# Kernel tuning notes

Hardware: AMD Instinct MI355X
Metric: run time of the kernel (lower is better)

Reference implementation:

```python
import jax, jax.numpy as jnp
import numpy as np

B, C, L = 4, 64, 4096
RED = 4          # reduction -> q/k channels = C // RED = 16
N_HASHES = 4
HASH_BUCKETS = min(L // 4, 32)  # = 32, matches torch code
EPS = 1e-5


def _conv1x1(x, W, b):
    # x: [B, Cin, L], W: [Cout, Cin], b: [Cout]
    return jnp.einsum('bcl,oc->bol', x, W) + b[None, :, None]


def setup_inputs() -> dict:
    key = jax.random.key(0)
    ks = jax.random.split(key, 12)
    Cq = C // RED
    x = jax.random.normal(ks[0], (B, C, L), dtype=jnp.float32)
    hash_idx = jax.random.randint(ks[1], (B, N_HASHES, L), 0, HASH_BUCKETS, dtype=jnp.int32)
    sC = 1.0 / np.sqrt(C)
    Wq = jax.random.normal(ks[2], (Cq, C), dtype=jnp.float32) * sC
    bq = jax.random.normal(ks[3], (Cq,), dtype=jnp.float32) * 0.01
    Wk = jax.random.normal(ks[4], (Cq, C), dtype=jnp.float32) * sC
    bk = jax.random.normal(ks[5], (Cq,), dtype=jnp.float32) * 0.01
    Wv = jax.random.normal(ks[6], (C, C), dtype=jnp.float32) * sC
    bv = jax.random.normal(ks[7], (C,), dtype=jnp.float32) * 0.01
    Wo = jax.random.normal(ks[8], (C, C), dtype=jnp.float32) * sC
    bo = jax.random.normal(ks[9], (C,), dtype=jnp.float32) * 0.01
    gamma = jax.random.normal(ks[10], (1,), dtype=jnp.float32)  # nonzero so attn path matters
    bn_w = jnp.ones((C,), dtype=jnp.float32)
    bn_b = jnp.zeros((C,), dtype=jnp.float32)
    return dict(x=x, hash_idx=hash_idx, Wq=Wq, bq=bq, Wk=Wk, bk=bk,
                Wv=Wv, bv=bv, Wo=Wo, bo=bo, gamma=gamma, bn_w=bn_w, bn_b=bn_b)


def reference(x, hash_idx, Wq, bq, Wk, bk, Wv, bv, Wo, bo, gamma, bn_w, bn_b):
    # 1x1 conv projections
    q = _conv1x1(x, Wq, bq)   # [B, C/RED, L]
    k = _conv1x1(x, Wk, bk)   # [B, C/RED, L]
    v = _conv1x1(x, Wv, bv)   # [B, C, L]

    qT = q.transpose(0, 2, 1)  # [B, L, Cq]
    kT = k.transpose(0, 2, 1)
    vT = v.transpose(0, 2, 1)  # [B, L, C]

    # raw scores are hash-independent; only the bucket mask changes per hash
    scores = jnp.einsum('bic,bjc->bij', qT, kT)  # [B, L, L], no sqrt(d) scaling (matches torch)

    n_hashes = hash_idx.shape[1]
    acc = jnp.zeros_like(vT)
    for h in range(n_hashes):  # small fixed loop
        idx = hash_idx[:, h, :]                       # [B, L]
        mask = idx[:, :, None] == idx[:, None, :]     # same-bucket mask [B, L, L]
        s = jnp.where(mask, scores, -1e9)
        attn = jax.nn.softmax(s, axis=-1)             # within-bucket softmax (diag always valid)
        acc = acc + jnp.einsum('bij,bjc->bic', attn, vT)
    attn_out = (acc / n_hashes).transpose(0, 2, 1)    # [B, C, L], averaged over hashes

    out = _conv1x1(attn_out, Wo, bo)
    out = gamma * out + x                             # residual with learned scalar

    # BatchNorm1d, training mode: biased batch stats over (B, L) per channel
    mean = out.mean(axis=(0, 2), keepdims=True)
    var = out.var(axis=(0, 2), keepdims=True)
    out = (out - mean) * jax.lax.rsqrt(var + EPS)
    out = out * bn_w[None, :, None] + bn_b[None, :, None]
    return out
```

## Files before the change

kernel.cpp:

```cpp
#include <hip/hip_runtime.h>
#include <math.h>

#define Bn 4
#define Cn 64
#define Ln 4096
#define CQ 16
#define NH 4
#define NB 32
#define EPSV 1e-5f

#define MAXS 384
#define CH2 64
#define KSTR 20
#define VSTR 64

#define QSZ   (Bn*Ln*CQ)
#define VSZ   (Bn*Ln*Cn)
#define ACCSZ (Bn*Ln*Cn)
#define NBH   (Bn*NH)

#define OFF_K   QSZ
#define OFF_V   (2*QSZ)
#define OFF_ACC (2*QSZ + VSZ)

#define LOG2E 1.44269504088896f

__global__ __launch_bounds__(256) void proj_kernel(
        const float* __restrict__ x,
        const float* __restrict__ Wq, const float* __restrict__ bq,
        const float* __restrict__ Wk, const float* __restrict__ bk,
        const float* __restrict__ Wv, const float* __restrict__ bv,
        float* __restrict__ q, float* __restrict__ k, float* __restrict__ v) {
    __shared__ float sWt[Cn*32];
    __shared__ float sb[32];
    int tid = threadIdx.x;
    int third = blockIdx.x % 3;
    int pg    = blockIdx.x / 3;
    int rbase = third * 32;
    for (int idx = tid; idx < Cn*32; idx += 256) {
        int rr = idx & 31, c = idx >> 5;
        int r = rbase + rr;
        float w;
        if (r < 16)      w = Wq[r*Cn + c];
        else if (r < 32) w = Wk[(r-16)*Cn + c];
        else             w = Wv[(r-32)*Cn + c];
        sWt[c*32 + rr] = w;
    }
    if (tid < 32) {
        int r = rbase + tid;
        sb[tid] = (r < 16) ? bq[r] : (r < 32 ? bk[r-16] : bv[r-32]);
    }
    __syncthreads();
    int p = tid & 63, og = tid >> 6;
    int gp = pg * 64 + p;
    int b = gp >> 12, l = gp & (Ln - 1);
    const float* xp = &x[b*Cn*Ln + l];
    int rr0 = og * 8;
    float val[8];
    #pragma unroll
    for (int i = 0; i < 8; i++) val[i] = sb[rr0 + i];
    #pragma unroll
    for (int c0 = 0; c0 < Cn; c0 += 8) {
        float xv[8];
        #pragma unroll
        for (int i = 0; i < 8; i++) xv[i] = xp[(c0 + i)*Ln];
        #pragma unroll
        for (int i = 0; i < 8; i++) {
            const float* wrow = &sWt[(c0 + i)*32 + rr0];
            #pragma unroll
            for (int j = 0; j < 8; j++) val[j] = fmaf(wrow[j], xv[i], val[j]);
        }
    }
    int f = third*8 + og*2;
    float4 t0 = make_float4(val[0], val[1], val[2], val[3]);
    float4 t1 = make_float4(val[4], val[5], val[6], val[7]);
    float4* q4 = (float4*)&q[gp*CQ];
    float4* k4 = (float4*)&k[gp*CQ];
    float4* v4 = (float4*)&v[gp*Cn];
    if (f < 4)      { q4[f]   = t0; q4[f+1] = t1; }
    else if (f < 8) { k4[f-4] = t0; k4[f-3] = t1; }
    else            { v4[f-8] = t0; v4[f-7] = t1; }
}

template<int NS, int MODE>
__device__ __forceinline__ void attn_pass(
        int qbase, int S, int b, int h, int tid, int rem,
        const int* list, float* ks, float* vs,
        const float* __restrict__ q, const float* __restrict__ k,
        const float* __restrict__ v, float* __restrict__ acc) {
    int qd = tid >> 2, c4 = tid & 3;
    float4 qr[NS][4];
    float4 o[NS][4];
    float lsum[NS];
    int qi[NS], iqr[NS];
    #pragma unroll
    for (int s = 0; s < NS; s++) {
        qi[s] = qbase + 64*s + qd;
        iqr[s] = 0;
        lsum[s] = 0.f;
        #pragma unroll
        for (int i = 0; i < 4; i++) o[s][i] = make_float4(0.f,0.f,0.f,0.f);
        if (qi[s] < S) {
            iqr[s] = list[qi[s]];
            const float4* qp = (const float4*)&q[(b*Ln + iqr[s])*CQ];
            #pragma unroll
            for (int i = 0; i < 4; i++) {
                float4 t = qp[i];
                t.x*=LOG2E; t.y*=LOG2E; t.z*=LOG2E; t.w*=LOG2E;
                qr[s][i] = t;
            }
        } else {
            #pragma unroll
            for (int i = 0; i < 4; i++) qr[s][i] = make_float4(0.f,0.f,0.f,0.f);
        }
    }
    for (int cc = 0; cc < S; cc += CH2) {
        int nk = min(CH2, S - cc);
        __syncthreads();
        {
            int jj = tid >> 2, cf = tid & 3;
            if (jj < nk) {
                const float4* kp = (const float4*)&k[(b*Ln + list[cc+jj])*CQ];
                *(float4*)&ks[jj*KSTR + cf*4] = kp[cf];
            }
        }
        #pragma unroll
        for (int uu = 0; uu < 4; uu++) {
            int idx = uu*256 + tid;
            int jj = idx >> 4, cf = idx & 15;
            if (jj < nk) {
                const float4* vp = (const float4*)&v[(b*Ln + list[cc+jj])*Cn];
                *(float4*)&vs[jj*VSTR + cf*4] = vp[cf];
            }
        }
        __syncthreads();
        if (rem > 0) {
            for (int j = 0; j < nk; j++) {
                const float4* kr = (const float4*)&ks[j*KSTR];
                float4 k0 = kr[0], k1 = kr[1], k2 = kr[2], k3 = kr[3];
                const float4* vp4 = (const float4*)&vs[j*VSTR + c4*16];
                float4 v0 = vp4[0], v1 = vp4[1], v2 = vp4[2], v3 = vp4[3];
                #pragma unroll
                for (int s = 0; s < NS; s++) {
                    float s0 = qr[s][0].x*k0.x + qr[s][0].y*k0.y + qr[s][0].z*k0.z + qr[s][0].w*k0.w;
                    float s1 = qr[s][1].x*k1.x + qr[s][1].y*k1.y + qr[s][1].z*k1.z + qr[s][1].w*k1.w;
                    float s2 = qr[s][2].x*k2.x + qr[s][2].y*k2.y + qr[s][2].z*k2.z + qr[s][2].w*k2.w;
                    float s3 = qr[s][3].x*k3.x + qr[s][3].y*k3.y + qr[s][3].z*k3.z + qr[s][3].w*k3.w;
                    float pw = __builtin_amdgcn_exp2f((s0 + s1) + (s2 + s3));
                    lsum[s] += pw;
                    o[s][0].x = fmaf(pw, v0.x, o[s][0].x); o[s][0].y = fmaf(pw, v0.y, o[s][0].y);
                    o[s][0].z = fmaf(pw, v0.z, o[s][0].z); o[s][0].w = fmaf(pw, v0.w, o[s][0].w);
                    o[s][1].x = fmaf(pw, v1.x, o[s][1].x); o[s][1].y = fmaf(pw, v1.y, o[s][1].y);
                    o[s][1].z = fmaf(pw, v1.z, o[s][1].z); o[s][1].w = fmaf(pw, v1.w, o[s][1].w);
                    o[s][2].x = fmaf(pw, v2.x, o[s][2].x); o[s][2].y = fmaf(pw, v2.y, o[s][2].y);
                    o[s][2].z = fmaf(pw, v2.z, o[s][2].z); o[s][2].w = fmaf(pw, v2.w, o[s][2].w);
                    o[s][3].x = fmaf(pw, v3.x, o[s][3].x); o[s][3].y = fmaf(pw, v3.y, o[s][3].y);
                    o[s][3].z = fmaf(pw, v3.z, o[s][3].z); o[s][3].w = fmaf(pw, v3.w, o[s][3].w);
                }
            }
        }
    }
    #pragma unroll
    for (int s = 0; s < NS; s++) {
        if (qi[s] < S) {
            float inv = 1.f / lsum[s];
            #pragma unroll
            for (int i = 0; i < 4; i++) {
                o[s][i].x*=inv; o[s][i].y*=inv; o[s][i].z*=inv; o[s][i].w*=inv;
            }
            if (MODE == 1) {
                float4* ap = (float4*)&acc[((size_t)h*Bn*Ln + b*Ln + iqr[s])*Cn + c4*16];
                ap[0]=o[s][0]; ap[1]=o[s][1]; ap[2]=o[s][2]; ap[3]=o[s][3];
            } else {
                float* ap = &acc[(b*Ln + iqr[s])*Cn + c4*16];
                #pragma unroll
                for (int i = 0; i < 4; i++) {
                    atomicAdd(&ap[4*i+0], (&o[s][i].x)[0]);
                    atomicAdd(&ap[4*i+1], (&o[s][i].x)[1]);
                    atomicAdd(&ap[4*i+2], (&o[s][i].x)[2]);
                    atomicAdd(&ap[4*i+3], (&o[s][i].x)[3]);
                }
            }
        }
    }
}

template<int MODE>
__global__ __launch_bounds__(256, 2) void attn_kernel(
        const float* __restrict__ q, const float* __restrict__ k,
        const float* __restrict__ v, const int* __restrict__ hidx,
        float* __restrict__ acc) {
    __shared__ int list[MAXS];
    __shared__ float ks[CH2*KSTR];
    __shared__ float vs[CH2*VSTR];
    __shared__ int wtot[4];
    int blk = blockIdx.x;
    int u  = blk & (NB-1);
    int bh = blk >> 5;
    int b  = bh >> 2;
    int h  = bh & 3;
    int tid = threadIdx.x;

    const int4* hp4 = (const int4*)(&hidx[bh*Ln] + tid*16);
    int hv[16];
    #pragma unroll
    for (int t = 0; t < 4; t++) {
        int4 tmp = hp4[t];
        hv[t*4+0]=tmp.x; hv[t*4+1]=tmp.y; hv[t*4+2]=tmp.z; hv[t*4+3]=tmp.w;
    }
    int myCnt = 0;
    #pragma unroll
    for (int t = 0; t < 16; t++) myCnt += (hv[t] == u);
    int lane = tid & 63, wv = tid >> 6;
    int pre = myCnt;
    #pragma unroll
    for (int d = 1; d < 64; d <<= 1) {
        int t = __shfl_up(pre, d, 64);
        if (lane >= d) pre += t;
    }
    if (lane == 63) wtot[wv] = pre;
    __syncthreads();
    int base = 0;
    #pragma unroll
    for (int w = 0; w < 4; w++) base += (w < wv) ? wtot[w] : 0;
    int Sall = wtot[0] + wtot[1] + wtot[2] + wtot[3];
    int S = min(Sall, MAXS);
    int excl = base + pre - myCnt;
    #pragma unroll
    for (int t = 0; t < 16; t++) {
        if (hv[t] == u) {
            if (excl < MAXS) list[excl] = tid*16 + t;
            excl++;
        }
    }
    __syncthreads();

    int wq0 = (tid >> 6) << 4;
    for (int qbase = 0; qbase < S; qbase += 192) {
        int rem = S - qbase - wq0;
        if (rem > 128)     attn_pass<3,MODE>(qbase,S,b,h,tid,rem,list,ks,vs,q,k,v,acc);
        else if (rem > 64) attn_pass<2,MODE>(qbase,S,b,h,tid,rem,list,ks,vs,q,k,v,acc);
        else               attn_pass<1,MODE>(qbase,S,b,h,tid,rem,list,ks,vs,q,k,v,acc);
    }
}

template<int MODE>
__global__ __launch_bounds__(256) void outconv_kernel(
        const float* __restrict__ acc, const float* __restrict__ Wo,
        const float* __restrict__ bo, const float* __restrict__ gamma,
        const float* __restrict__ x, float* __restrict__ y) {
    __shared__ float sWt[Cn*32];
    __shared__ float sb[32];
    int tid = threadIdx.x;
    int half = blockIdx.x & 1;
    int pg   = blockIdx.x >> 1;
    for (int idx = tid; idx < Cn*32; idx += 256) {
        int oo = idx & 31, c = idx >> 5;
        sWt[c*32 + oo] = Wo[(half*32 + oo)*Cn + c];
    }
    if (tid < 32) sb[tid] = bo[half*32 + tid];
    __syncthreads();
    float g = gamma[0];
    int p = tid & 63, og = tid >> 6;
    int gp = pg * 64 + p;
    int b = gp >> 12, l = gp & (Ln - 1);
    int oo0 = og * 8;
    float val[8];
    #pragma unroll
    for (int i = 0; i < 8; i++) val[i] = sb[oo0 + i];
    const float4* ap0 = (const float4*)&acc[(size_t)gp*Cn];
    #pragma unroll
    for (int c4 = 0; c4 < 16; c4++) {
        float4 t = ap0[c4];
        if (MODE == 1) {
            float4 t1 = ap0[(size_t)ACCSZ/4   + c4];
            float4 t2 = ap0[(size_t)ACCSZ/4*2 + c4];
            float4 t3 = ap0[(size_t)ACCSZ/4*3 + c4];
            t.x += t1.x + t2.x + t3.x; t.y += t1.y + t2.y + t3.y;
            t.z += t1.z + t2.z + t3.z; t.w += t1.w + t2.w + t3.w;
        }
        float a0 = t.x*0.25f, a1 = t.y*0.25f, a2 = t.z*0.25f, a3 = t.w*0.25f;
        const float* w0 = &sWt[(c4*4+0)*32 + oo0];
        const float* w1 = &sWt[(c4*4+1)*32 + oo0];
        const float* w2 = &sWt[(c4*4+2)*32 + oo0];
        const float* w3 = &sWt[(c4*4+3)*32 + oo0];
        #pragma unroll
        for (int i = 0; i < 8; i++) {
            val[i] = fmaf(w0[i], a0, val[i]);
            val[i] = fmaf(w1[i], a1, val[i]);
            val[i] = fmaf(w2[i], a2, val[i]);
            val[i] = fmaf(w3[i], a3, val[i]);
        }
    }
    #pragma unroll
    for (int i = 0; i < 8; i++) {
        int o = half*32 + oo0 + i;
        float yv = fmaf(g, val[i], x[(b*Cn + o)*Ln + l]);
        y[(b*Cn + o)*Ln + l] = yv;
    }
}

__global__ __launch_bounds__(256) void stats_kernel(
        const float* __restrict__ y, float* __restrict__ ssum, float* __restrict__ ssq) {
    int c = blockIdx.x >> 2;
    int part = blockIdx.x & 3;
    int tid = threadIdx.x;
    const float4* yp = (const float4*)&y[(part*Cn + c)*Ln];
    float s = 0.f, s2 = 0.f;
    #pragma unroll
    for (int i = 0; i < 4; i++) {
        float4 t = yp[i*256 + tid];
        s  += t.x + t.y + t.z + t.w;
        s2 += t.x*t.x + t.y*t.y + t.z*t.z + t.w*t.w;
    }
    #pragma unroll
    for (int w = 1; w < 64; w <<= 1) {
        s  += __shfl_xor(s,  w, 64);
        s2 += __shfl_xor(s2, w, 64);
    }
    __shared__ float rs[4], rs2[4];
    int wv = tid >> 6;
    if ((tid & 63) == 0) { rs[wv] = s; rs2[wv] = s2; }
    __syncthreads();
    if (tid == 0) {
        atomicAdd(&ssum[c], rs[0]+rs[1]+rs[2]+rs[3]);
        atomicAdd(&ssq[c],  rs2[0]+rs2[1]+rs2[2]+rs2[3]);
    }
}

__global__ __launch_bounds__(256) void norm_kernel(
        const float* __restrict__ y,
        const float* __restrict__ ssum, const float* __restrict__ ssq,
        const float* __restrict__ bnw, const float* __restrict__ bnb,
        float* __restrict__ out) {
    int idx = blockIdx.x * 256 + threadIdx.x;
    int flat = idx * 4;
    int c = (flat / Ln) & 63;
    const float n = (float)(Bn*Ln);
    float mu = ssum[c] / n;
    float var = ssq[c] / n - mu*mu;
    float is = rsqrtf(var + EPSV);
    float w = is * bnw[c];
    float bb = bnb[c] - mu * w;
    float4 t = ((const float4*)y)[idx];
    float4 r;
    r.x = t.x*w + bb; r.y = t.y*w + bb; r.z = t.z*w + bb; r.w = t.w*w + bb;
    ((float4*)out)[idx] = r;
}

extern "C" void kernel_launch(void* const* d_in, const int* in_sizes, int n_in,
                              void* d_out, int out_size, void* d_ws, size_t ws_size,
                              hipStream_t stream) {
    const float* x    = (const float*)d_in[0];
    const int*   hidx = (const int*)  d_in[1];
    const float* Wq   = (const float*)d_in[2];
    const float* bq   = (const float*)d_in[3];
    const float* Wk   = (const float*)d_in[4];
    const float* bk   = (const float*)d_in[5];
    const float* Wv   = (const float*)d_in[6];
    const float* bv   = (const float*)d_in[7];
    const float* Wo   = (const float*)d_in[8];
    const float* bo   = (const float*)d_in[9];
    const float* gam  = (const float*)d_in[10];
    const float* bnw  = (const float*)d_in[11];
    const float* bnb  = (const float*)d_in[12];
    float* out = (float*)d_out;

    float* ws  = (float*)d_ws;
    float* q   = ws;
    float* k   = ws + OFF_K;
    float* v   = ws + OFF_V;
    float* acc = ws + OFF_ACC;
    float* y   = ws;

    const size_t bigNeed = ((size_t)OFF_ACC + 4*(size_t)ACCSZ + 2*Cn) * sizeof(float);
    bool big = ws_size >= bigNeed;
    float* ssum = acc + (big ? 4*(size_t)ACCSZ : (size_t)ACCSZ);
    float* ssq  = ssum + Cn;

    hipMemsetAsync(ssum, 0, 2*Cn*sizeof(float), stream);

    proj_kernel<<<Bn*Ln/64*3, 256, 0, stream>>>(x, Wq, bq, Wk, bk, Wv, bv, q, k, v);
    if (big) {
        attn_kernel<1><<<NBH*NB, 256, 0, stream>>>(q, k, v, hidx, acc);
        outconv_kernel<1><<<Bn*Ln/64*2, 256, 0, stream>>>(acc, Wo, bo, gam, x, y);
    } else {
        hipMemsetAsync(acc, 0, (size_t)ACCSZ*sizeof(float), stream);
        attn_kernel<0><<<NBH*NB, 256, 0, stream>>>(q, k, v, hidx, acc);
        outconv_kernel<0><<<Bn*Ln/64*2, 256, 0, stream>>>(acc, Wo, bo, gam, x, y);
    }
    stats_kernel<<<Cn*4, 256, 0, stream>>>(y, ssum, ssq);
    norm_kernel<<<Bn*Cn*Ln/4/256, 256, 0, stream>>>(y, ssum, ssq, bnw, bnb, out);
}
```

Baseline: 182.2 us.

## Split bucket queries across two blocks and read K/V directly from global memory

The attention kernel now launches twice as many blocks, with each bucket's query list split into interleaved halves. The shared-memory K/V staging and its barriers are removed, and every thread streams K and V rows straight from global memory (relying on the cache). Occupancy is raised to 4 blocks per CU. In exchange, each block rebuilds the bucket list, global K/V traffic is duplicated across the two halves, and the inner loop now depends on cache latency instead of LDS.

```diff
diff --git a/kernel.cpp b/kernel.cpp
--- a/kernel.cpp
+++ b/kernel.cpp
@@ -10,9 +10,7 @@
 #define EPSV 1e-5f
 
 #define MAXS 384
-#define CH2 64
-#define KSTR 20
-#define VSTR 64
+#define QS 2
 
 #define QSZ   (Bn*Ln*CQ)
 #define VSZ   (Bn*Ln*Cn)
@@ -83,26 +81,28 @@
 }
 
 template<int NS, int MODE>
-__device__ __forceinline__ void attn_pass(
-        int qbase, int S, int b, int h, int tid, int rem,
-        const int* list, float* ks, float* vs,
+__device__ __forceinline__ void attn_sweep(
+        int qs, int cnt, int S, int b, int h, int tid,
+        const int* list,
         const float* __restrict__ q, const float* __restrict__ k,
         const float* __restrict__ v, float* __restrict__ acc) {
     int qd = tid >> 2, c4 = tid & 3;
+    const float* kb = &k[(size_t)b*Ln*CQ];
+    const float* vb = &v[(size_t)b*Ln*Cn + c4*16];
     float4 qr[NS][4];
     float4 o[NS][4];
     float lsum[NS];
-    int qi[NS], iqr[NS];
+    int m[NS], iqr[NS];
     #pragma unroll
     for (int s = 0; s < NS; s++) {
-        qi[s] = qbase + 64*s + qd;
+        m[s] = qd + 64*s;
         iqr[s] = 0;
         lsum[s] = 0.f;
         #pragma unroll
         for (int i = 0; i < 4; i++) o[s][i] = make_float4(0.f,0.f,0.f,0.f);
-        if (qi[s] < S) {
-            iqr[s] = list[qi[s]];
-            const float4* qp = (const float4*)&q[(b*Ln + iqr[s])*CQ];
+        if (m[s] < cnt) {
+            iqr[s] = list[qs + QS*m[s]];
+            const float4* qp = (const float4*)&q[((size_t)b*Ln + iqr[s])*CQ];
             #pragma unroll
             for (int i = 0; i < 4; i++) {
                 float4 t = qp[i];
@@ -114,55 +114,33 @@
             for (int i = 0; i < 4; i++) qr[s][i] = make_float4(0.f,0.f,0.f,0.f);
         }
     }
-    for (int cc = 0; cc < S; cc += CH2) {
-        int nk = min(CH2, S - cc);
-        __syncthreads();
-        {
-            int jj = tid >> 2, cf = tid & 3;
-            if (jj < nk) {
-                const float4* kp = (const float4*)&k[(b*Ln + list[cc+jj])*CQ];
-                *(float4*)&ks[jj*KSTR + cf*4] = kp[cf];
-            }
-        }
-        #pragma unroll
-        for (int uu = 0; uu < 4; uu++) {
-            int idx = uu*256 + tid;
-            int jj = idx >> 4, cf = idx & 15;
-            if (jj < nk) {
-                const float4* vp = (const float4*)&v[(b*Ln + list[cc+jj])*Cn];
-                *(float4*)&vs[jj*VSTR + cf*4] = vp[cf];
-            }
-        }
-        __syncthreads();
-        if (rem > 0) {
-            for (int j = 0; j < nk; j++) {
-                const float4* kr = (const float4*)&ks[j*KSTR];
-                float4 k0 = kr[0], k1 = kr[1], k2 = kr[2], k3 = kr[3];
-                const float4* vp4 = (const float4*)&vs[j*VSTR + c4*16];
-                float4 v0 = vp4[0], v1 = vp4[1], v2 = vp4[2], v3 = vp4[3];
-                #pragma unroll
-                for (int s = 0; s < NS; s++) {
-                    float s0 = qr[s][0].x*k0.x + qr[s][0].y*k0.y + qr[s][0].z*k0.z + qr[s][0].w*k0.w;
-                    float s1 = qr[s][1].x*k1.x + qr[s][1].y*k1.y + qr[s][1].z*k1.z + qr[s][1].w*k1.w;
-                    float s2 = qr[s][2].x*k2.x + qr[s][2].y*k2.y + qr[s][2].z*k2.z + qr[s][2].w*k2.w;
-                    float s3 = qr[s][3].x*k3.x + qr[s][3].y*k3.y + qr[s][3].z*k3.z + qr[s][3].w*k3.w;
-                    float pw = __builtin_amdgcn_exp2f((s0 + s1) + (s2 + s3));
-                    lsum[s] += pw;
-                    o[s][0].x = fmaf(pw, v0.x, o[s][0].x); o[s][0].y = fmaf(pw, v0.y, o[s][0].y);
-                    o[s][0].z = fmaf(pw, v0.z, o[s][0].z); o[s][0].w = fmaf(pw, v0.w, o[s][0].w);
-                    o[s][1].x = fmaf(pw, v1.x, o[s][1].x); o[s][1].y = fmaf(pw, v1.y, o[s][1].y);
-                    o[s][1].z = fmaf(pw, v1.z, o[s][1].z); o[s][1].w = fmaf(pw, v1.w, o[s][1].w);
-                    o[s][2].x = fmaf(pw, v2.x, o[s][2].x); o[s][2].y = fmaf(pw, v2.y, o[s][2].y);
-                    o[s][2].z = fmaf(pw, v2.z, o[s][2].z); o[s][2].w = fmaf(pw, v2.w, o[s][2].w);
-                    o[s][3].x = fmaf(pw, v3.x, o[s][3].x); o[s][3].y = fmaf(pw, v3.y, o[s][3].y);
-                    o[s][3].z = fmaf(pw, v3.z, o[s][3].z); o[s][3].w = fmaf(pw, v3.w, o[s][3].w);
-                }
-            }
+    for (int j = 0; j < S; j++) {
+        int jl = list[j];
+        const float4* kp = (const float4*)&kb[jl*CQ];
+        float4 k0 = kp[0], k1 = kp[1], k2 = kp[2], k3 = kp[3];
+        const float4* vp = (const float4*)&vb[jl*Cn];
+        float4 v0 = vp[0], v1 = vp[1], v2 = vp[2], v3 = vp[3];
+        #pragma unroll
+        for (int s = 0; s < NS; s++) {
+            float s0 = qr[s][0].x*k0.x + qr[s][0].y*k0.y + qr[s][0].z*k0.z + qr[s][0].w*k0.w;
+            float s1 = qr[s][1].x*k1.x + qr[s][1].y*k1.y + qr[s][1].z*k1.z + qr[s][1].w*k1.w;
+            float s2 = qr[s][2].x*k2.x + qr[s][2].y*k2.y + qr[s][2].z*k2.z + qr[s][2].w*k2.w;
+            float s3 = qr[s][3].x*k3.x + qr[s][3].y*k3.y + qr[s][3].z*k3.z + qr[s][3].w*k3.w;
+            float pw = __builtin_amdgcn_exp2f((s0 + s1) + (s2 + s3));
+            lsum[s] += pw;
+            o[s][0].x = fmaf(pw, v0.x, o[s][0].x); o[s][0].y = fmaf(pw, v0.y, o[s][0].y);
+            o[s][0].z = fmaf(pw, v0.z, o[s][0].z); o[s][0].w = fmaf(pw, v0.w, o[s][0].w);
+            o[s][1].x = fmaf(pw, v1.x, o[s][1].x); o[s][1].y = fmaf(pw, v1.y, o[s][1].y);
+            o[s][1].z = fmaf(pw, v1.z, o[s][1].z); o[s][1].w = fmaf(pw, v1.w, o[s][1].w);
+            o[s][2].x = fmaf(pw, v2.x, o[s][2].x); o[s][2].y = fmaf(pw, v2.y, o[s][2].y);
+            o[s][2].z = fmaf(pw, v2.z, o[s][2].z); o[s][2].w = fmaf(pw, v2.w, o[s][2].w);
+            o[s][3].x = fmaf(pw, v3.x, o[s][3].x); o[s][3].y = fmaf(pw, v3.y, o[s][3].y);
+            o[s][3].z = fmaf(pw, v3.z, o[s][3].z); o[s][3].w = fmaf(pw, v3.w, o[s][3].w);
         }
     }
     #pragma unroll
     for (int s = 0; s < NS; s++) {
-        if (qi[s] < S) {
+        if (m[s] < cnt) {
             float inv = 1.f / lsum[s];
             #pragma unroll
             for (int i = 0; i < 4; i++) {
@@ -172,7 +150,7 @@
                 float4* ap = (float4*)&acc[((size_t)h*Bn*Ln + b*Ln + iqr[s])*Cn + c4*16];
                 ap[0]=o[s][0]; ap[1]=o[s][1]; ap[2]=o[s][2]; ap[3]=o[s][3];
             } else {
-                float* ap = &acc[(b*Ln + iqr[s])*Cn + c4*16];
+                float* ap = &acc[((size_t)b*Ln + iqr[s])*Cn + c4*16];
                 #pragma unroll
                 for (int i = 0; i < 4; i++) {
                     atomicAdd(&ap[4*i+0], (&o[s][i].x)[0]);
@@ -186,17 +164,17 @@
 }
 
 template<int MODE>
-__global__ __launch_bounds__(256, 2) void attn_kernel(
+__global__ __launch_bounds__(256, 4) void attn_kernel(
         const float* __restrict__ q, const float* __restrict__ k,
         const float* __restrict__ v, const int* __restrict__ hidx,
         float* __restrict__ acc) {
     __shared__ int list[MAXS];
-    __shared__ float ks[CH2*KSTR];
-    __shared__ float vs[CH2*VSTR];
     __shared__ int wtot[4];
     int blk = blockIdx.x;
-    int u  = blk & (NB-1);
-    int bh = blk >> 5;
+    int qs  = blk & 1;
+    int rest = blk >> 1;
+    int u  = rest & (NB-1);
+    int bh = rest >> 5;
     int b  = bh >> 2;
     int h  = bh & 3;
     int tid = threadIdx.x;
@@ -236,12 +214,11 @@
     __syncthreads();
 
     int wq0 = (tid >> 6) << 4;
-    for (int qbase = 0; qbase < S; qbase += 192) {
-        int rem = S - qbase - wq0;
-        if (rem > 128)     attn_pass<3,MODE>(qbase,S,b,h,tid,rem,list,ks,vs,q,k,v,acc);
-        else if (rem > 64) attn_pass<2,MODE>(qbase,S,b,h,tid,rem,list,ks,vs,q,k,v,acc);
-        else               attn_pass<1,MODE>(qbase,S,b,h,tid,rem,list,ks,vs,q,k,v,acc);
-    }
+    int cnt = (S + 1 - qs) >> 1;
+    int rem = cnt - wq0;
+    if (rem > 128)     attn_sweep<3,MODE>(qs,cnt,S,b,h,tid,list,q,k,v,acc);
+    else if (rem > 64) attn_sweep<2,MODE>(qs,cnt,S,b,h,tid,list,q,k,v,acc);
+    else if (rem > 0)  attn_sweep<1,MODE>(qs,cnt,S,b,h,tid,list,q,k,v,acc);
 }
 
 template<int MODE>
@@ -382,11 +359,11 @@
 
     proj_kernel<<<Bn*Ln/64*3, 256, 0, stream>>>(x, Wq, bq, Wk, bk, Wv, bv, q, k, v);
     if (big) {
-        attn_kernel<1><<<NBH*NB, 256, 0, stream>>>(q, k, v, hidx, acc);
+        attn_kernel<1><<<NBH*NB*QS, 256, 0, stream>>>(q, k, v, hidx, acc);
         outconv_kernel<1><<<Bn*Ln/64*2, 256, 0, stream>>>(acc, Wo, bo, gam, x, y);
     } else {
         hipMemsetAsync(acc, 0, (size_t)ACCSZ*sizeof(float), stream);
-        attn_kernel<0><<<NBH*NB, 256, 0, stream>>>(q, k, v, hidx, acc);
+        attn_kernel<0><<<NBH*NB*QS, 256, 0, stream>>>(q, k, v, hidx, acc);
         outconv_kernel<0><<<Bn*Ln/64*2, 256, 0, stream>>>(acc, Wo, bo, gam, x, y);
     }
     stats_kernel<<<Cn*4, 256, 0, stream>>>(y, ssum, ssq);
```

Result: slower. 253.1 us (+38.9%).

## Split attention key range across two blocks with atomic partial sums

Applied to the files above, without the earlier changes.

Each (batch, hash, bucket) attention block is split into two blocks that each handle half of the bucket's keys. Unnormalized outputs and softmax denominators are accumulated with atomics into the per-hash buffers, and normalization moves into the output-conv kernel. Launch bounds are raised to 4 blocks per CU. The goal is more parallelism and occupancy for the 512-block attention launch, at the cost of an extra memset of the large accumulator, many float atomics, and a denominator buffer read.

```diff
diff --git a/kernel.cpp b/kernel.cpp
--- a/kernel.cpp
+++ b/kernel.cpp
@@ -18,6 +18,7 @@
 #define VSZ   (Bn*Ln*Cn)
 #define ACCSZ (Bn*Ln*Cn)
 #define NBH   (Bn*NH)
+#define LSUMSZ (NH*Bn*Ln)
 
 #define OFF_K   QSZ
 #define OFF_V   (2*QSZ)
@@ -84,10 +85,11 @@
 
 template<int NS, int MODE>
 __device__ __forceinline__ void attn_pass(
-        int qbase, int S, int b, int h, int tid, int rem,
+        int qbase, int S, int j0, int j1, int b, int h, int tid,
         const int* list, float* ks, float* vs,
         const float* __restrict__ q, const float* __restrict__ k,
-        const float* __restrict__ v, float* __restrict__ acc) {
+        const float* __restrict__ v, float* __restrict__ acc,
+        float* __restrict__ lsumBuf) {
     int qd = tid >> 2, c4 = tid & 3;
     float4 qr[NS][4];
     float4 o[NS][4];
@@ -102,7 +104,7 @@
         for (int i = 0; i < 4; i++) o[s][i] = make_float4(0.f,0.f,0.f,0.f);
         if (qi[s] < S) {
             iqr[s] = list[qi[s]];
-            const float4* qp = (const float4*)&q[(b*Ln + iqr[s])*CQ];
+            const float4* qp = (const float4*)&q[((size_t)b*Ln + iqr[s])*CQ];
             #pragma unroll
             for (int i = 0; i < 4; i++) {
                 float4 t = qp[i];
@@ -114,13 +116,13 @@
             for (int i = 0; i < 4; i++) qr[s][i] = make_float4(0.f,0.f,0.f,0.f);
         }
     }
-    for (int cc = 0; cc < S; cc += CH2) {
-        int nk = min(CH2, S - cc);
+    for (int cc = j0; cc < j1; cc += CH2) {
+        int nk = min(CH2, j1 - cc);
         __syncthreads();
         {
             int jj = tid >> 2, cf = tid & 3;
             if (jj < nk) {
-                const float4* kp = (const float4*)&k[(b*Ln + list[cc+jj])*CQ];
+                const float4* kp = (const float4*)&k[((size_t)b*Ln + list[cc+jj])*CQ];
                 *(float4*)&ks[jj*KSTR + cf*4] = kp[cf];
             }
         }
@@ -129,50 +131,56 @@
             int idx = uu*256 + tid;
             int jj = idx >> 4, cf = idx & 15;
             if (jj < nk) {
-                const float4* vp = (const float4*)&v[(b*Ln + list[cc+jj])*Cn];
+                const float4* vp = (const float4*)&v[((size_t)b*Ln + list[cc+jj])*Cn];
                 *(float4*)&vs[jj*VSTR + cf*4] = vp[cf];
             }
         }
         __syncthreads();
-        if (rem > 0) {
-            for (int j = 0; j < nk; j++) {
-                const float4* kr = (const float4*)&ks[j*KSTR];
-                float4 k0 = kr[0], k1 = kr[1], k2 = kr[2], k3 = kr[3];
-                const float4* vp4 = (const float4*)&vs[j*VSTR + c4*16];
-                float4 v0 = vp4[0], v1 = vp4[1], v2 = vp4[2], v3 = vp4[3];
-                #pragma unroll
-                for (int s = 0; s < NS; s++) {
-                    float s0 = qr[s][0].x*k0.x + qr[s][0].y*k0.y + qr[s][0].z*k0.z + qr[s][0].w*k0.w;
-                    float s1 = qr[s][1].x*k1.x + qr[s][1].y*k1.y + qr[s][1].z*k1.z + qr[s][1].w*k1.w;
-                    float s2 = qr[s][2].x*k2.x + qr[s][2].y*k2.y + qr[s][2].z*k2.z + qr[s][2].w*k2.w;
-                    float s3 = qr[s][3].x*k3.x + qr[s][3].y*k3.y + qr[s][3].z*k3.z + qr[s][3].w*k3.w;
-                    float pw = __builtin_amdgcn_exp2f((s0 + s1) + (s2 + s3));
-                    lsum[s] += pw;
-                    o[s][0].x = fmaf(pw, v0.x, o[s][0].x); o[s][0].y = fmaf(pw, v0.y, o[s][0].y);
-                    o[s][0].z = fmaf(pw, v0.z, o[s][0].z); o[s][0].w = fmaf(pw, v0.w, o[s][0].w);
-                    o[s][1].x = fmaf(pw, v1.x, o[s][1].x); o[s][1].y = fmaf(pw, v1.y, o[s][1].y);
-                    o[s][1].z = fmaf(pw, v1.z, o[s][1].z); o[s][1].w = fmaf(pw, v1.w, o[s][1].w);
-                    o[s][2].x = fmaf(pw, v2.x, o[s][2].x); o[s][2].y = fmaf(pw, v2.y, o[s][2].y);
-                    o[s][2].z = fmaf(pw, v2.z, o[s][2].z); o[s][2].w = fmaf(pw, v2.w, o[s][2].w);
-                    o[s][3].x = fmaf(pw, v3.x, o[s][3].x); o[s][3].y = fmaf(pw, v3.y, o[s][3].y);
-                    o[s][3].z = fmaf(pw, v3.z, o[s][3].z); o[s][3].w = fmaf(pw, v3.w, o[s][3].w);
-                }
+        for (int j = 0; j < nk; j++) {
+            const float4* kr = (const float4*)&ks[j*KSTR];
+            float4 k0 = kr[0], k1 = kr[1], k2 = kr[2], k3 = kr[3];
+            const float4* vp4 = (const float4*)&vs[j*VSTR + c4*16];
+            float4 v0 = vp4[0], v1 = vp4[1], v2 = vp4[2], v3 = vp4[3];
+            #pragma unroll
+            for (int s = 0; s < NS; s++) {
+                float s0 = qr[s][0].x*k0.x + qr[s][0].y*k0.y + qr[s][0].z*k0.z + qr[s][0].w*k0.w;
+                float s1 = qr[s][1].x*k1.x + qr[s][1].y*k1.y + qr[s][1].z*k1.z + qr[s][1].w*k1.w;
+                float s2 = qr[s][2].x*k2.x + qr[s][2].y*k2.y + qr[s][2].z*k2.z + qr[s][2].w*k2.w;
+                float s3 = qr[s][3].x*k3.x + qr[s][3].y*k3.y + qr[s][3].z*k3.z + qr[s][3].w*k3.w;
+                float pw = __builtin_amdgcn_exp2f((s0 + s1) + (s2 + s3));
+                lsum[s] += pw;
+                o[s][0].x = fmaf(pw, v0.x, o[s][0].x); o[s][0].y = fmaf(pw, v0.y, o[s][0].y);
+                o[s][0].z = fmaf(pw, v0.z, o[s][0].z); o[s][0].w = fmaf(pw, v0.w, o[s][0].w);
+                o[s][1].x = fmaf(pw, v1.x, o[s][1].x); o[s][1].y = fmaf(pw, v1.y, o[s][1].y);
+                o[s][1].z = fmaf(pw, v1.z, o[s][1].z); o[s][1].w = fmaf(pw, v1.w, o[s][1].w);
+                o[s][2].x = fmaf(pw, v2.x, o[s][2].x); o[s][2].y = fmaf(pw, v2.y, o[s][2].y);
+                o[s][2].z = fmaf(pw, v2.z, o[s][2].z); o[s][2].w = fmaf(pw, v2.w, o[s][2].w);
+                o[s][3].x = fmaf(pw, v3.x, o[s][3].x); o[s][3].y = fmaf(pw, v3.y, o[s][3].y);
+                o[s][3].z = fmaf(pw, v3.z, o[s][3].z); o[s][3].w = fmaf(pw, v3.w, o[s][3].w);
             }
         }
     }
     #pragma unroll
     for (int s = 0; s < NS; s++) {
         if (qi[s] < S) {
-            float inv = 1.f / lsum[s];
-            #pragma unroll
-            for (int i = 0; i < 4; i++) {
-                o[s][i].x*=inv; o[s][i].y*=inv; o[s][i].z*=inv; o[s][i].w*=inv;
-            }
             if (MODE == 1) {
-                float4* ap = (float4*)&acc[((size_t)h*Bn*Ln + b*Ln + iqr[s])*Cn + c4*16];
-                ap[0]=o[s][0]; ap[1]=o[s][1]; ap[2]=o[s][2]; ap[3]=o[s][3];
+                float* ap = &acc[((size_t)h*Bn*Ln + b*Ln + iqr[s])*Cn + c4*16];
+                #pragma unroll
+                for (int i = 0; i < 4; i++) {
+                    atomicAdd(&ap[4*i+0], (&o[s][i].x)[0]);
+                    atomicAdd(&ap[4*i+1], (&o[s][i].x)[1]);
+                    atomicAdd(&ap[4*i+2], (&o[s][i].x)[2]);
+                    atomicAdd(&ap[4*i+3], (&o[s][i].x)[3]);
+                }
+                if (c4 == 0)
+                    atomicAdd(&lsumBuf[(size_t)h*Bn*Ln + b*Ln + iqr[s]], lsum[s]);
             } else {
-                float* ap = &acc[(b*Ln + iqr[s])*Cn + c4*16];
+                float inv = 1.f / lsum[s];
+                #pragma unroll
+                for (int i = 0; i < 4; i++) {
+                    o[s][i].x*=inv; o[s][i].y*=inv; o[s][i].z*=inv; o[s][i].w*=inv;
+                }
+                float* ap = &acc[((size_t)b*Ln + iqr[s])*Cn + c4*16];
                 #pragma unroll
                 for (int i = 0; i < 4; i++) {
                     atomicAdd(&ap[4*i+0], (&o[s][i].x)[0]);
@@ -186,17 +194,19 @@
 }
 
 template<int MODE>
-__global__ __launch_bounds__(256, 2) void attn_kernel(
+__global__ __launch_bounds__(256, 4) void attn_kernel(
         const float* __restrict__ q, const float* __restrict__ k,
         const float* __restrict__ v, const int* __restrict__ hidx,
-        float* __restrict__ acc) {
+        float* __restrict__ acc, float* __restrict__ lsumBuf) {
     __shared__ int list[MAXS];
     __shared__ float ks[CH2*KSTR];
     __shared__ float vs[CH2*VSTR];
     __shared__ int wtot[4];
     int blk = blockIdx.x;
-    int u  = blk & (NB-1);
-    int bh = blk >> 5;
+    int half = 0, rest = blk;
+    if (MODE == 1) { half = blk & 1; rest = blk >> 1; }
+    int u  = rest & (NB-1);
+    int bh = rest >> 5;
     int b  = bh >> 2;
     int h  = bh & 3;
     int tid = threadIdx.x;
@@ -235,20 +245,25 @@
     }
     __syncthreads();
 
+    int halfS = (S + 1) >> 1;
+    int j0 = (MODE == 1) ? half * halfS : 0;
+    int j1 = (MODE == 1) ? min(S, j0 + halfS) : S;
+
     int wq0 = (tid >> 6) << 4;
     for (int qbase = 0; qbase < S; qbase += 192) {
         int rem = S - qbase - wq0;
-        if (rem > 128)     attn_pass<3,MODE>(qbase,S,b,h,tid,rem,list,ks,vs,q,k,v,acc);
-        else if (rem > 64) attn_pass<2,MODE>(qbase,S,b,h,tid,rem,list,ks,vs,q,k,v,acc);
-        else               attn_pass<1,MODE>(qbase,S,b,h,tid,rem,list,ks,vs,q,k,v,acc);
+        if (rem > 128)     attn_pass<3,MODE>(qbase,S,j0,j1,b,h,tid,list,ks,vs,q,k,v,acc,lsumBuf);
+        else if (rem > 64) attn_pass<2,MODE>(qbase,S,j0,j1,b,h,tid,list,ks,vs,q,k,v,acc,lsumBuf);
+        else               attn_pass<1,MODE>(qbase,S,j0,j1,b,h,tid,list,ks,vs,q,k,v,acc,lsumBuf);
     }
 }
 
 template<int MODE>
 __global__ __launch_bounds__(256) void outconv_kernel(
-        const float* __restrict__ acc, const float* __restrict__ Wo,
-        const float* __restrict__ bo, const float* __restrict__ gamma,
-        const float* __restrict__ x, float* __restrict__ y) {
+        const float* __restrict__ acc, const float* __restrict__ lsumBuf,
+        const float* __restrict__ Wo, const float* __restrict__ bo,
+        const float* __restrict__ gamma, const float* __restrict__ x,
+        float* __restrict__ y) {
     __shared__ float sWt[Cn*32];
     __shared__ float sb[32];
     int tid = threadIdx.x;
@@ -268,18 +283,30 @@
     float val[8];
     #pragma unroll
     for (int i = 0; i < 8; i++) val[i] = sb[oo0 + i];
+    float linv[4];
+    if (MODE == 1) {
+        #pragma unroll
+        for (int hh = 0; hh < 4; hh++)
+            linv[hh] = 0.25f / lsumBuf[(size_t)hh*Bn*Ln + gp];
+    }
     const float4* ap0 = (const float4*)&acc[(size_t)gp*Cn];
     #pragma unroll
     for (int c4 = 0; c4 < 16; c4++) {
-        float4 t = ap0[c4];
+        float4 t;
         if (MODE == 1) {
+            float4 t0 = ap0[c4];
             float4 t1 = ap0[(size_t)ACCSZ/4   + c4];
             float4 t2 = ap0[(size_t)ACCSZ/4*2 + c4];
             float4 t3 = ap0[(size_t)ACCSZ/4*3 + c4];
-            t.x += t1.x + t2.x + t3.x; t.y += t1.y + t2.y + t3.y;
-            t.z += t1.z + t2.z + t3.z; t.w += t1.w + t2.w + t3.w;
-        }
-        float a0 = t.x*0.25f, a1 = t.y*0.25f, a2 = t.z*0.25f, a3 = t.w*0.25f;
+            t.x = t0.x*linv[0] + t1.x*linv[1] + t2.x*linv[2] + t3.x*linv[3];
+            t.y = t0.y*linv[0] + t1.y*linv[1] + t2.y*linv[2] + t3.y*linv[3];
+            t.z = t0.z*linv[0] + t1.z*linv[1] + t2.z*linv[2] + t3.z*linv[3];
+            t.w = t0.w*linv[0] + t1.w*linv[1] + t2.w*linv[2] + t3.w*linv[3];
+        } else {
+            float4 t0 = ap0[c4];
+            t.x = t0.x*0.25f; t.y = t0.y*0.25f; t.z = t0.z*0.25f; t.w = t0.w*0.25f;
+        }
+        float a0 = t.x, a1 = t.y, a2 = t.z, a3 = t.w;
         const float* w0 = &sWt[(c4*4+0)*32 + oo0];
         const float* w1 = &sWt[(c4*4+1)*32 + oo0];
         const float* w2 = &sWt[(c4*4+2)*32 + oo0];
@@ -373,21 +400,22 @@
     float* acc = ws + OFF_ACC;
     float* y   = ws;
 
-    const size_t bigNeed = ((size_t)OFF_ACC + 4*(size_t)ACCSZ + 2*Cn) * sizeof(float);
+    const size_t bigNeed = ((size_t)OFF_ACC + 4*(size_t)ACCSZ + LSUMSZ + 2*Cn) * sizeof(float);
     bool big = ws_size >= bigNeed;
-    float* ssum = acc + (big ? 4*(size_t)ACCSZ : (size_t)ACCSZ);
-    float* ssq  = ssum + Cn;
+    float* lsumB = acc + (big ? 4*(size_t)ACCSZ : (size_t)ACCSZ);
+    float* ssum  = lsumB + (big ? LSUMSZ : 0);
+    float* ssq   = ssum + Cn;
 
     hipMemsetAsync(ssum, 0, 2*Cn*sizeof(float), stream);
-
     proj_kernel<<<Bn*Ln/64*3, 256, 0, stream>>>(x, Wq, bq, Wk, bk, Wv, bv, q, k, v);
     if (big) {
-        attn_kernel<1><<<NBH*NB, 256, 0, stream>>>(q, k, v, hidx, acc);
-        outconv_kernel<1><<<Bn*Ln/64*2, 256, 0, stream>>>(acc, Wo, bo, gam, x, y);
+        hipMemsetAsync(acc, 0, (4*(size_t)ACCSZ + LSUMSZ)*sizeof(float), stream);
+        attn_kernel<1><<<NBH*NB*2, 256, 0, stream>>>(q, k, v, hidx, acc, lsumB);
+        outconv_kernel<1><<<Bn*Ln/64*2, 256, 0, stream>>>(acc, lsumB, Wo, bo, gam, x, y);
     } else {
         hipMemsetAsync(acc, 0, (size_t)ACCSZ*sizeof(float), stream);
-        attn_kernel<0><<<NBH*NB, 256, 0, stream>>>(q, k, v, hidx, acc);
-        outconv_kernel<0><<<Bn*Ln/64*2, 256, 0, stream>>>(acc, Wo, bo, gam, x, y);
+        attn_kernel<0><<<NBH*NB, 256, 0, stream>>>(q, k, v, hidx, acc, lsumB);
+        outconv_kernel<0><<<Bn*Ln/64*2, 256, 0, stream>>>(acc, lsumB, Wo, bo, gam, x, y);
     }
     stats_kernel<<<Cn*4, 256, 0, stream>>>(y, ssum, ssq);
     norm_kernel<<<Bn*Cn*Ln/4/256, 256, 0, stream>>>(y, ssum, ssq, bnw, bnb, out);
```

Result: slower. 635.8 us (+249.0%).

## Split attention value channels across two blocks and drop stats atomics/memset

Applied to the files above, without the earlier changes.

Each attention block now handles half of the 64 value channels, doubling the grid to 1024 blocks. This halves per-thread accumulators and shared V tile size, so launch bounds can target 4 blocks per SIMD. The cost is that q·k scores and exp2 are computed twice, once per half. Separately, the BN stats kernel writes per-block partial sums instead of atomics, so the memset is gone, and norm_kernel sums the 4 partials itself.

```diff
diff --git a/kernel.cpp b/kernel.cpp
--- a/kernel.cpp
+++ b/kernel.cpp
@@ -12,7 +12,7 @@
 #define MAXS 384
 #define CH2 64
 #define KSTR 20
-#define VSTR 64
+#define VSTR2 36
 
 #define QSZ   (Bn*Ln*CQ)
 #define VSZ   (Bn*Ln*Cn)
@@ -84,13 +84,13 @@
 
 template<int NS, int MODE>
 __device__ __forceinline__ void attn_pass(
-        int qbase, int S, int b, int h, int tid, int rem,
+        int qbase, int S, int b, int h, int half, int tid,
         const int* list, float* ks, float* vs,
         const float* __restrict__ q, const float* __restrict__ k,
         const float* __restrict__ v, float* __restrict__ acc) {
     int qd = tid >> 2, c4 = tid & 3;
     float4 qr[NS][4];
-    float4 o[NS][4];
+    float4 o[NS][2];
     float lsum[NS];
     int qi[NS], iqr[NS];
     #pragma unroll
@@ -98,11 +98,11 @@
         qi[s] = qbase + 64*s + qd;
         iqr[s] = 0;
         lsum[s] = 0.f;
-        #pragma unroll
-        for (int i = 0; i < 4; i++) o[s][i] = make_float4(0.f,0.f,0.f,0.f);
+        o[s][0] = make_float4(0.f,0.f,0.f,0.f);
+        o[s][1] = make_float4(0.f,0.f,0.f,0.f);
         if (qi[s] < S) {
             iqr[s] = list[qi[s]];
-            const float4* qp = (const float4*)&q[(b*Ln + iqr[s])*CQ];
+            const float4* qp = (const float4*)&q[((size_t)b*Ln + iqr[s])*CQ];
             #pragma unroll
             for (int i = 0; i < 4; i++) {
                 float4 t = qp[i];
@@ -120,43 +120,37 @@
         {
             int jj = tid >> 2, cf = tid & 3;
             if (jj < nk) {
-                const float4* kp = (const float4*)&k[(b*Ln + list[cc+jj])*CQ];
+                const float4* kp = (const float4*)&k[((size_t)b*Ln + list[cc+jj])*CQ];
                 *(float4*)&ks[jj*KSTR + cf*4] = kp[cf];
             }
         }
         #pragma unroll
-        for (int uu = 0; uu < 4; uu++) {
+        for (int uu = 0; uu < 2; uu++) {
             int idx = uu*256 + tid;
-            int jj = idx >> 4, cf = idx & 15;
+            int jj = idx >> 3, cf = idx & 7;
             if (jj < nk) {
-                const float4* vp = (const float4*)&v[(b*Ln + list[cc+jj])*Cn];
-                *(float4*)&vs[jj*VSTR + cf*4] = vp[cf];
+                const float4* vp = (const float4*)&v[((size_t)b*Ln + list[cc+jj])*Cn + half*32];
+                *(float4*)&vs[jj*VSTR2 + cf*4] = vp[cf];
             }
         }
         __syncthreads();
-        if (rem > 0) {
-            for (int j = 0; j < nk; j++) {
-                const float4* kr = (const float4*)&ks[j*KSTR];
-                float4 k0 = kr[0], k1 = kr[1], k2 = kr[2], k3 = kr[3];
-                const float4* vp4 = (const float4*)&vs[j*VSTR + c4*16];
-                float4 v0 = vp4[0], v1 = vp4[1], v2 = vp4[2], v3 = vp4[3];
-                #pragma unroll
-                for (int s = 0; s < NS; s++) {
-                    float s0 = qr[s][0].x*k0.x + qr[s][0].y*k0.y + qr[s][0].z*k0.z + qr[s][0].w*k0.w;
-                    float s1 = qr[s][1].x*k1.x + qr[s][1].y*k1.y + qr[s][1].z*k1.z + qr[s][1].w*k1.w;
-                    float s2 = qr[s][2].x*k2.x + qr[s][2].y*k2.y + qr[s][2].z*k2.z + qr[s][2].w*k2.w;
-                    float s3 = qr[s][3].x*k3.x + qr[s][3].y*k3.y + qr[s][3].z*k3.z + qr[s][3].w*k3.w;
-                    float pw = __builtin_amdgcn_exp2f((s0 + s1) + (s2 + s3));
-                    lsum[s] += pw;
-                    o[s][0].x = fmaf(pw, v0.x, o[s][0].x); o[s][0].y = fmaf(pw, v0.y, o[s][0].y);
-                    o[s][0].z = fmaf(pw, v0.z, o[s][0].z); o[s][0].w = fmaf(pw, v0.w, o[s][0].w);
-                    o[s][1].x = fmaf(pw, v1.x, o[s][1].x); o[s][1].y = fmaf(pw, v1.y, o[s][1].y);
-                    o[s][1].z = fmaf(pw, v1.z, o[s][1].z); o[s][1].w = fmaf(pw, v1.w, o[s][1].w);
-                    o[s][2].x = fmaf(pw, v2.x, o[s][2].x); o[s][2].y = fmaf(pw, v2.y, o[s][2].y);
-                    o[s][2].z = fmaf(pw, v2.z, o[s][2].z); o[s][2].w = fmaf(pw, v2.w, o[s][2].w);
-                    o[s][3].x = fmaf(pw, v3.x, o[s][3].x); o[s][3].y = fmaf(pw, v3.y, o[s][3].y);
-                    o[s][3].z = fmaf(pw, v3.z, o[s][3].z); o[s][3].w = fmaf(pw, v3.w, o[s][3].w);
-                }
+        for (int j = 0; j < nk; j++) {
+            const float4* kr = (const float4*)&ks[j*KSTR];
+            float4 k0 = kr[0], k1 = kr[1], k2 = kr[2], k3 = kr[3];
+            const float4* vp4 = (const float4*)&vs[j*VSTR2 + c4*8];
+            float4 v0 = vp4[0], v1 = vp4[1];
+            #pragma unroll
+            for (int s = 0; s < NS; s++) {
+                float s0 = qr[s][0].x*k0.x + qr[s][0].y*k0.y + qr[s][0].z*k0.z + qr[s][0].w*k0.w;
+                float s1 = qr[s][1].x*k1.x + qr[s][1].y*k1.y + qr[s][1].z*k1.z + qr[s][1].w*k1.w;
+                float s2 = qr[s][2].x*k2.x + qr[s][2].y*k2.y + qr[s][2].z*k2.z + qr[s][2].w*k2.w;
+                float s3 = qr[s][3].x*k3.x + qr[s][3].y*k3.y + qr[s][3].z*k3.z + qr[s][3].w*k3.w;
+                float pw = __builtin_amdgcn_exp2f((s0 + s1) + (s2 + s3));
+                lsum[s] += pw;
+                o[s][0].x = fmaf(pw, v0.x, o[s][0].x); o[s][0].y = fmaf(pw, v0.y, o[s][0].y);
+                o[s][0].z = fmaf(pw, v0.z, o[s][0].z); o[s][0].w = fmaf(pw, v0.w, o[s][0].w);
+                o[s][1].x = fmaf(pw, v1.x, o[s][1].x); o[s][1].y = fmaf(pw, v1.y, o[s][1].y);
+                o[s][1].z = fmaf(pw, v1.z, o[s][1].z); o[s][1].w = fmaf(pw, v1.w, o[s][1].w);
             }
         }
     }
@@ -164,39 +158,36 @@
     for (int s = 0; s < NS; s++) {
         if (qi[s] < S) {
             float inv = 1.f / lsum[s];
-            #pragma unroll
-            for (int i = 0; i < 4; i++) {
-                o[s][i].x*=inv; o[s][i].y*=inv; o[s][i].z*=inv; o[s][i].w*=inv;
-            }
+            o[s][0].x*=inv; o[s][0].y*=inv; o[s][0].z*=inv; o[s][0].w*=inv;
+            o[s][1].x*=inv; o[s][1].y*=inv; o[s][1].z*=inv; o[s][1].w*=inv;
             if (MODE == 1) {
-                float4* ap = (float4*)&acc[((size_t)h*Bn*Ln + b*Ln + iqr[s])*Cn + c4*16];
-                ap[0]=o[s][0]; ap[1]=o[s][1]; ap[2]=o[s][2]; ap[3]=o[s][3];
+                float4* ap = (float4*)&acc[((size_t)h*Bn*Ln + b*Ln + iqr[s])*Cn + half*32 + c4*8];
+                ap[0] = o[s][0]; ap[1] = o[s][1];
             } else {
-                float* ap = &acc[(b*Ln + iqr[s])*Cn + c4*16];
-                #pragma unroll
-                for (int i = 0; i < 4; i++) {
-                    atomicAdd(&ap[4*i+0], (&o[s][i].x)[0]);
-                    atomicAdd(&ap[4*i+1], (&o[s][i].x)[1]);
-                    atomicAdd(&ap[4*i+2], (&o[s][i].x)[2]);
-                    atomicAdd(&ap[4*i+3], (&o[s][i].x)[3]);
-                }
+                float* ap = &acc[((size_t)b*Ln + iqr[s])*Cn + half*32 + c4*8];
+                atomicAdd(&ap[0], o[s][0].x); atomicAdd(&ap[1], o[s][0].y);
+                atomicAdd(&ap[2], o[s][0].z); atomicAdd(&ap[3], o[s][0].w);
+                atomicAdd(&ap[4], o[s][1].x); atomicAdd(&ap[5], o[s][1].y);
+                atomicAdd(&ap[6], o[s][1].z); atomicAdd(&ap[7], o[s][1].w);
             }
         }
     }
 }
 
 template<int MODE>
-__global__ __launch_bounds__(256, 2) void attn_kernel(
+__global__ __launch_bounds__(256, 4) void attn_kernel(
         const float* __restrict__ q, const float* __restrict__ k,
         const float* __restrict__ v, const int* __restrict__ hidx,
         float* __restrict__ acc) {
     __shared__ int list[MAXS];
     __shared__ float ks[CH2*KSTR];
-    __shared__ float vs[CH2*VSTR];
+    __shared__ float vs[CH2*VSTR2];
     __shared__ int wtot[4];
     int blk = blockIdx.x;
-    int u  = blk & (NB-1);
-    int bh = blk >> 5;
+    int half = blk & 1;
+    int rest = blk >> 1;
+    int u  = rest & (NB-1);
+    int bh = rest >> 5;
     int b  = bh >> 2;
     int h  = bh & 3;
     int tid = threadIdx.x;
@@ -238,9 +229,9 @@
     int wq0 = (tid >> 6) << 4;
     for (int qbase = 0; qbase < S; qbase += 192) {
         int rem = S - qbase - wq0;
-        if (rem > 128)     attn_pass<3,MODE>(qbase,S,b,h,tid,rem,list,ks,vs,q,k,v,acc);
-        else if (rem > 64) attn_pass<2,MODE>(qbase,S,b,h,tid,rem,list,ks,vs,q,k,v,acc);
-        else               attn_pass<1,MODE>(qbase,S,b,h,tid,rem,list,ks,vs,q,k,v,acc);
+        if (rem > 128)     attn_pass<3,MODE>(qbase,S,b,h,half,tid,list,ks,vs,q,k,v,acc);
+        else if (rem > 64) attn_pass<2,MODE>(qbase,S,b,h,half,tid,list,ks,vs,q,k,v,acc);
+        else               attn_pass<1,MODE>(qbase,S,b,h,half,tid,list,ks,vs,q,k,v,acc);
     }
 }
 
@@ -301,7 +292,7 @@
 }
 
 __global__ __launch_bounds__(256) void stats_kernel(
-        const float* __restrict__ y, float* __restrict__ ssum, float* __restrict__ ssq) {
+        const float* __restrict__ y, float* __restrict__ ssumP, float* __restrict__ ssqP) {
     int c = blockIdx.x >> 2;
     int part = blockIdx.x & 3;
     int tid = threadIdx.x;
@@ -323,22 +314,25 @@
     if ((tid & 63) == 0) { rs[wv] = s; rs2[wv] = s2; }
     __syncthreads();
     if (tid == 0) {
-        atomicAdd(&ssum[c], rs[0]+rs[1]+rs[2]+rs[3]);
-        atomicAdd(&ssq[c],  rs2[0]+rs2[1]+rs2[2]+rs2[3]);
+        ssumP[blockIdx.x] = rs[0]+rs[1]+rs[2]+rs[3];
+        ssqP[blockIdx.x]  = rs2[0]+rs2[1]+rs2[2]+rs2[3];
     }
 }
 
 __global__ __launch_bounds__(256) void norm_kernel(
         const float* __restrict__ y,
-        const float* __restrict__ ssum, const float* __restrict__ ssq,
+        const float* __restrict__ ssumP, const float* __restrict__ ssqP,
         const float* __restrict__ bnw, const float* __restrict__ bnb,
         float* __restrict__ out) {
     int idx = blockIdx.x * 256 + threadIdx.x;
     int flat = idx * 4;
     int c = (flat / Ln) & 63;
+    float s = 0.f, s2 = 0.f;
+    #pragma unroll
+    for (int hh = 0; hh < 4; hh++) { s += ssumP[c*4+hh]; s2 += ssqP[c*4+hh]; }
     const float n = (float)(Bn*Ln);
-    float mu = ssum[c] / n;
-    float var = ssq[c] / n - mu*mu;
+    float mu = s / n;
+    float var = s2 / n - mu*mu;
     float is = rsqrtf(var + EPSV);
     float w = is * bnw[c];
     float bb = bnb[c] - mu * w;
@@ -373,22 +367,20 @@
     float* acc = ws + OFF_ACC;
     float* y   = ws;
 
-    const size_t bigNeed = ((size_t)OFF_ACC + 4*(size_t)ACCSZ + 2*Cn) * sizeof(float);
+    const size_t bigNeed = ((size_t)OFF_ACC + 4*(size_t)ACCSZ + 512) * sizeof(float);
     bool big = ws_size >= bigNeed;
-    float* ssum = acc + (big ? 4*(size_t)ACCSZ : (size_t)ACCSZ);
-    float* ssq  = ssum + Cn;
-
-    hipMemsetAsync(ssum, 0, 2*Cn*sizeof(float), stream);
+    float* ssumP = acc + (big ? 4*(size_t)ACCSZ : (size_t)ACCSZ);
+    float* ssqP  = ssumP + 256;
 
     proj_kernel<<<Bn*Ln/64*3, 256, 0, stream>>>(x, Wq, bq, Wk, bk, Wv, bv, q, k, v);
     if (big) {
-        attn_kernel<1><<<NBH*NB, 256, 0, stream>>>(q, k, v, hidx, acc);
+        attn_kernel<1><<<NBH*NB*2, 256, 0, stream>>>(q, k, v, hidx, acc);
         outconv_kernel<1><<<Bn*Ln/64*2, 256, 0, stream>>>(acc, Wo, bo, gam, x, y);
     } else {
         hipMemsetAsync(acc, 0, (size_t)ACCSZ*sizeof(float), stream);
-        attn_kernel<0><<<NBH*NB, 256, 0, stream>>>(q, k, v, hidx, acc);
+        attn_kernel<0><<<NBH*NB*2, 256, 0, stream>>>(q, k, v, hidx, acc);
         outconv_kernel<0><<<Bn*Ln/64*2, 256, 0, stream>>>(acc, Wo, bo, gam, x, y);
     }
-    stats_kernel<<<Cn*4, 256, 0, stream>>>(y, ssum, ssq);
-    norm_kernel<<<Bn*Cn*Ln/4/256, 256, 0, stream>>>(y, ssum, ssq, bnw, bnb, out);
-}
+    stats_kernel<<<Cn*4, 256, 0, stream>>>(y, ssumP, ssqP);
+    norm_kernel<<<Bn*Cn*Ln/4/256, 256, 0, stream>>>(y, ssumP, ssqP, bnw, bnb, out);
+}
```

New measurement: 190.1 us. 4.3% more time.
